# Performance work log

Hardware: AMD Instinct MI355X
Metric: run time of the kernel (lower is better)

The kernel has to match this reference:

```python
import jax, jax.numpy as jnp
import numpy as np


def feature_map(x):
    # phi(x) = elu(x) + 1 (ensures positivity)
    return jax.nn.elu(x) + 1.0


def setup_inputs() -> dict:
    key = jax.random.key(0)
    k0, k1, k2, k3 = jax.random.split(key, 4)
    B, T, d_model, D = 4, 4096, 1024, 128
    x = jax.random.normal(k0, (B, T, d_model), dtype=jnp.float32)
    s = 1.0 / np.sqrt(d_model)
    Wq = jax.random.normal(k1, (d_model, D), dtype=jnp.float32) * s
    Wk = jax.random.normal(k2, (d_model, D), dtype=jnp.float32) * s
    Wv = jax.random.normal(k3, (d_model, D), dtype=jnp.float32) * s
    return {"x": x, "Wq": Wq, "Wk": Wk, "Wv": Wv}


def _causal_linear_attention(phi_q, phi_k, v):
    # phi_q, phi_k: [B,T,D]; v: [B,T,Dv]
    B, T, D = phi_q.shape
    Dv = v.shape[-1]
    # time-major for scan: [T,B,D]
    qT = jnp.swapaxes(phi_q, 0, 1)
    kT = jnp.swapaxes(phi_k, 0, 1)
    vT = jnp.swapaxes(v, 0, 1)

    def step(carry, inp):
        kv, ks = carry                       # kv: [B,D,Dv], ks: [B,D]
        qt, kt, vt = inp                     # each [B,D] / [B,Dv]
        kv = kv + kt[:, :, None] * vt[:, None, :]   # k_t^T v_t outer product
        ks = ks + kt
        num = jnp.einsum('bd,bdv->bv', qt, kv)      # [B,Dv]
        den = jnp.einsum('bd,bd->b', qt, ks)[:, None]
        return (kv, ks), num / den

    init = (jnp.zeros((B, D, Dv), phi_q.dtype), jnp.zeros((B, D), phi_q.dtype))
    _, outT = jax.lax.scan(step, init, (qT, kT, vT))  # outT: [T,B,Dv]
    return jnp.swapaxes(outT, 0, 1)


def reference(x, Wq, Wk, Wv):
    q = x @ Wq
    k = x @ Wk
    v = x @ Wv
    phi_q = feature_map(q)
    phi_k = feature_map(k)
    # dropout is identity in eval mode
    return _causal_linear_attention(phi_q, phi_k, v)
```

## Files before the change

### kernel.cpp

```cpp
#include <hip/hip_runtime.h>

#define DMODEL 1024
#define DHEAD 128
#define CHUNK 128
#define NCHUNK 32

typedef __attribute__((ext_vector_type(4))) float f32x4;
typedef __attribute__((ext_vector_type(8))) short bf16x8;

__device__ __forceinline__ unsigned short f2bf(float f) {
  union { float f; unsigned u; } v; v.f = f;
  unsigned r = v.u + 0x7FFF + ((v.u >> 16) & 1);
  return (unsigned short)(r >> 16);
}
__device__ __forceinline__ float bf2f(unsigned short h) {
  union { unsigned u; float f; } v; v.u = ((unsigned)h) << 16;
  return v.f;
}
__device__ __forceinline__ unsigned cvtpk(float lo, float hi) {
  unsigned r;
  asm("v_cvt_pk_bf16_f32 %0, %1, %2" : "=v"(r) : "v"(lo), "v"(hi));
  return r;
}
__device__ __forceinline__ void gload16(const void* g, void* l) {
  __builtin_amdgcn_global_load_lds(
      (const __attribute__((address_space(1))) unsigned int*)g,
      (__attribute__((address_space(3))) unsigned int*)l, 16, 0, 0);
}

__global__ __launch_bounds__(256) void transpose_w_kernel(
    const float* __restrict__ Wq, const float* __restrict__ Wk,
    const float* __restrict__ Wv, unsigned short* __restrict__ WT) {
  int id = blockIdx.x * 256 + threadIdx.x;
  int w = id >> 17;
  int rem = id & 131071;
  int n = rem >> 10;
  int k = rem & 1023;
  const float* W = (w == 0) ? Wq : (w == 1) ? Wk : Wv;
  WT[id] = f2bf(W[(size_t)k * DHEAD + n]);
}

__global__ __launch_bounds__(256) void proj_kernel(
    const float* __restrict__ x, const unsigned short* __restrict__ WT,
    unsigned short* __restrict__ phiQ, unsigned short* __restrict__ phiK,
    unsigned short* __restrict__ Vb) {
  const int bid = blockIdx.x;
  const int xcd = bid & 7;
  const int slot = bid >> 3;
  const int n0 = (slot & 1) << 6;
  const int m0 = ((xcd << 6) | (slot >> 1)) << 5;

  __shared__ float xs[32][64];
  __shared__ unsigned short wl[3][64][64];

  const int tid = threadIdx.x;
  const int wave = tid >> 6;
  const int lane = tid & 63;
  const int lrow = lane & 15, kgrp = lane >> 4;

  f32x4 acc[3][2];
#pragma unroll
  for (int w3 = 0; w3 < 3; ++w3)
#pragma unroll
    for (int mi = 0; mi < 2; ++mi) acc[w3][mi] = (f32x4)0.0f;

  for (int kk = 0; kk < DMODEL; kk += 64) {
    if (kk) __syncthreads();
#pragma unroll
    for (int i = 0; i < 2; ++i) {
      int instr = i * 4 + wave;
      int row = instr * 4 + (lane >> 4);
      int slotc = lane & 15;
      int gcol = (slotc ^ (row & 7)) << 2;
      gload16(&x[(size_t)(m0 + row) * DMODEL + kk + gcol],
              (char*)xs + instr * 1024);
    }
#pragma unroll
    for (int i = 0; i < 6; ++i) {
      int j = i * 4 + wave;
      int w3 = j >> 3;
      int jj = j & 7;
      int row = jj * 8 + (lane >> 3);
      int slotc = lane & 7;
      int gcol = (slotc ^ (row & 7)) << 3;
      gload16(&WT[(size_t)w3 * (DHEAD * DMODEL) + (size_t)(n0 + row) * DMODEL + kk + gcol],
              (char*)wl + w3 * 8192 + jj * 1024);
    }
    __syncthreads();

#pragma unroll
    for (int ks2 = 0; ks2 < 2; ++ks2) {
      bf16x8 af[2];
#pragma unroll
      for (int mi = 0; mi < 2; ++mi) {
        int arow = mi * 16 + lrow;
        int s0 = ks2 * 8 + kgrp * 2;
        const float4 f0 = *reinterpret_cast<const float4*>(
            &xs[arow][(s0 ^ (arow & 7)) << 2]);
        const float4 f1 = *reinterpret_cast<const float4*>(
            &xs[arow][((s0 + 1) ^ (arow & 7)) << 2]);
        union { unsigned u[4]; bf16x8 v; } p;
        p.u[0] = cvtpk(f0.x, f0.y);
        p.u[1] = cvtpk(f0.z, f0.w);
        p.u[2] = cvtpk(f1.x, f1.y);
        p.u[3] = cvtpk(f1.z, f1.w);
        af[mi] = p.v;
      }
#pragma unroll
      for (int w3 = 0; w3 < 3; ++w3) {
        int brow = wave * 16 + lrow;
        int bs = ks2 * 4 + kgrp;
        bf16x8 bf = *reinterpret_cast<const bf16x8*>(
            &wl[w3][brow][(bs ^ (brow & 7)) << 3]);
#pragma unroll
        for (int mi = 0; mi < 2; ++mi)
          acc[w3][mi] = __builtin_amdgcn_mfma_f32_16x16x32_bf16(af[mi], bf, acc[w3][mi], 0, 0, 0);
      }
    }
  }
#pragma unroll
  for (int w3 = 0; w3 < 3; ++w3) {
    unsigned short* outp = (w3 == 0) ? phiQ : (w3 == 1) ? phiK : Vb;
#pragma unroll
    for (int mi = 0; mi < 2; ++mi)
#pragma unroll
      for (int r = 0; r < 4; ++r) {
        int row = m0 + mi * 16 + kgrp * 4 + r;
        int col = n0 + wave * 16 + lrow;
        float v = acc[w3][mi][r];
        if (w3 < 2) v = (v > 0.0f) ? (v + 1.0f) : __expf(v);
        outp[(size_t)row * DHEAD + col] = f2bf(v);
      }
  }
}

__global__ __launch_bounds__(256) void chunkkv_kernel(
    const unsigned short* __restrict__ phiK, const unsigned short* __restrict__ Vb,
    float* __restrict__ KVc, float* __restrict__ ksc) {
  const int c = blockIdx.x;
  const int yv = blockIdx.y;
  const size_t base = (size_t)c * CHUNK * DHEAD;
  __shared__ unsigned short kt[128][136];
  __shared__ unsigned short vt[64][136];
  __shared__ float csum[2][128];
  const int tid = threadIdx.x;
  const int wave = tid >> 6, lane = tid & 63;
  const int lrow = lane & 15, kgrp = lane >> 4;

  {
    int t = tid & 127, dp = tid >> 7;
#pragma unroll
    for (int i = 0; i < 8; ++i) {
      int d0 = (dp + 2 * i) * 8;
      uint4 k4 = *reinterpret_cast<const uint4*>(&phiK[base + (size_t)t * DHEAD + d0]);
      const unsigned short* kp = reinterpret_cast<const unsigned short*>(&k4);
#pragma unroll
      for (int j = 0; j < 8; ++j) kt[d0 + j][t] = kp[j];
    }
#pragma unroll
    for (int i = 0; i < 4; ++i) {
      int dl = (dp + 2 * i) * 8;
      uint4 v4 = *reinterpret_cast<const uint4*>(
          &Vb[base + (size_t)t * DHEAD + yv * 64 + dl]);
      const unsigned short* vp = reinterpret_cast<const unsigned short*>(&v4);
#pragma unroll
      for (int j = 0; j < 8; ++j) vt[dl + j][t] = vp[j];
    }
  }
  __syncthreads();

  f32x4 acc[8];
#pragma unroll
  for (int j = 0; j < 8; ++j) acc[j] = (f32x4)0.0f;
#pragma unroll
  for (int ks = 0; ks < 4; ++ks) {
    int t0 = ks * 32 + kgrp * 8;
    bf16x8 afrag = *reinterpret_cast<const bf16x8*>(&vt[wave * 16 + lrow][t0]);
#pragma unroll
    for (int tc = 0; tc < 8; ++tc) {
      bf16x8 bfrag = *reinterpret_cast<const bf16x8*>(&kt[tc * 16 + lrow][t0]);
      acc[tc] = __builtin_amdgcn_mfma_f32_16x16x32_bf16(afrag, bfrag, acc[tc], 0, 0, 0);
    }
  }
  float* KVout = KVc + (size_t)c * (DHEAD * DHEAD);
#pragma unroll
  for (int tc = 0; tc < 8; ++tc)
#pragma unroll
    for (int r = 0; r < 4; ++r) {
      int dv = yv * 64 + wave * 16 + kgrp * 4 + r;
      int d = tc * 16 + lrow;
      KVout[dv * DHEAD + d] = acc[tc][r];
    }
  if (yv == 0) {
    int d = tid & 127, hh = tid >> 7;
    float s = 0.0f;
    for (int t = hh * 64; t < hh * 64 + 64; ++t) s += bf2f(kt[d][t]);
    csum[hh][d] = s;
    __syncthreads();
    if (tid < 128) ksc[(size_t)c * DHEAD + tid] = csum[0][tid] + csum[1][tid];
  }
}

__global__ __launch_bounds__(256) void prefix_kernel(
    const float* __restrict__ KVc, const float* __restrict__ ksc,
    unsigned short* __restrict__ KVp, float* __restrict__ ksp) {
  if (blockIdx.x < 256) {
    int id = blockIdx.x * 256 + threadIdx.x;
    int b = id >> 14;
    int e = id & 16383;
    size_t base = (size_t)b * NCHUNK * 16384 + e;
    float acc = 0.0f;
    for (int c = 0; c < NCHUNK; ++c) {
      KVp[base + (size_t)c * 16384] = f2bf(acc);
      acc += KVc[base + (size_t)c * 16384];
    }
  } else {
    for (int i = threadIdx.x; i < 512; i += 256) {
      int b = i >> 7, d = i & 127;
      size_t base = (size_t)b * NCHUNK * DHEAD + d;
      float acc = 0.0f;
      for (int c = 0; c < NCHUNK; ++c) {
        ksp[base + (size_t)c * DHEAD] = acc;
        acc += ksc[base + (size_t)c * DHEAD];
      }
    }
  }
}

__global__ __launch_bounds__(256) void out_kernel(
    const unsigned short* __restrict__ phiQ, const unsigned short* __restrict__ phiK,
    const unsigned short* __restrict__ Vb, const unsigned short* __restrict__ KVp,
    const float* __restrict__ ksp, float* __restrict__ outp) {
  const int c = blockIdx.x;
  const int h = blockIdx.y;
  const size_t kvbase = (size_t)c * CHUNK * DHEAD;
  const size_t qbase = kvbase + (size_t)h * 64 * DHEAD;
  __shared__ unsigned short qb[64][136];
  __shared__ unsigned short kb[128][136];
  __shared__ unsigned short vt[128][136];
  __shared__ float dsum[4][64];
  __shared__ float ks_l[128];
  const int tid = threadIdx.x;
  const int wave = tid >> 6, lane = tid & 63;
  const int lrow = lane & 15, kgrp = lane >> 4;

#pragma unroll
  for (int it = 0; it < 4; ++it) {
    int idx = it * 256 + tid;
    int t = idx >> 4;
    int d0 = (idx & 15) << 3;
    *reinterpret_cast<uint4*>(&qb[t][d0]) =
        *reinterpret_cast<const uint4*>(&phiQ[qbase + (size_t)t * DHEAD + d0]);
  }
  if (tid < 128) ks_l[tid] = ksp[(size_t)c * DHEAD + tid];
  if (h == 0) {
#pragma unroll
    for (int it = 0; it < 4; ++it) {
      int idx = it * 256 + tid;
      int t = idx >> 4;
      int d0 = (idx & 15) << 3;
      *reinterpret_cast<uint4*>(&kb[t][d0]) =
          *reinterpret_cast<const uint4*>(&phiK[kvbase + (size_t)t * DHEAD + d0]);
    }
    int t = tid & 63, dp = tid >> 6;
#pragma unroll
    for (int i = 0; i < 4; ++i) {
      int d0 = (dp + 4 * i) * 8;
      uint4 v4 = *reinterpret_cast<const uint4*>(&Vb[kvbase + (size_t)t * DHEAD + d0]);
      const unsigned short* vp = reinterpret_cast<const unsigned short*>(&v4);
#pragma unroll
      for (int j = 0; j < 8; ++j) vt[d0 + j][t] = vp[j];
    }
  } else {
#pragma unroll
    for (int it = 0; it < 8; ++it) {
      int idx = it * 256 + tid;
      int t = idx >> 4;
      int d0 = (idx & 15) << 3;
      *reinterpret_cast<uint4*>(&kb[t][d0]) =
          *reinterpret_cast<const uint4*>(&phiK[kvbase + (size_t)t * DHEAD + d0]);
    }
    int t = tid & 127, dp = tid >> 7;
#pragma unroll
    for (int i = 0; i < 8; ++i) {
      int d0 = (dp + 2 * i) * 8;
      uint4 v4 = *reinterpret_cast<const uint4*>(&Vb[kvbase + (size_t)t * DHEAD + d0]);
      const unsigned short* vp = reinterpret_cast<const unsigned short*>(&v4);
#pragma unroll
      for (int j = 0; j < 8; ++j) vt[d0 + j][t] = vp[j];
    }
  }
  __syncthreads();

  if (h == 0) {
    f32x4 sa[4];
#pragma unroll
    for (int i = 0; i < 4; ++i) sa[i] = (f32x4)0.0f;
#pragma unroll
    for (int ks = 0; ks < 4; ++ks) {
      int d0 = ks * 32 + kgrp * 8;
      bf16x8 af = *reinterpret_cast<const bf16x8*>(&qb[wave * 16 + lrow][d0]);
#pragma unroll
      for (int tc = 0; tc < 4; ++tc) {
        bf16x8 bf = *reinterpret_cast<const bf16x8*>(&kb[tc * 16 + lrow][d0]);
        sa[tc] = __builtin_amdgcn_mfma_f32_16x16x32_bf16(af, bf, sa[tc], 0, 0, 0);
      }
    }
    __syncthreads();
#pragma unroll
    for (int tc = 0; tc < 4; ++tc)
#pragma unroll
      for (int r = 0; r < 4; ++r) {
        int trow = wave * 16 + kgrp * 4 + r;
        int s = tc * 16 + lrow;
        kb[trow][s] = f2bf((s <= trow) ? sa[tc][r] : 0.0f);
      }
  } else {
    f32x4 sa[8];
#pragma unroll
    for (int i = 0; i < 8; ++i) sa[i] = (f32x4)0.0f;
#pragma unroll
    for (int ks = 0; ks < 4; ++ks) {
      int d0 = ks * 32 + kgrp * 8;
      bf16x8 af = *reinterpret_cast<const bf16x8*>(&qb[wave * 16 + lrow][d0]);
#pragma unroll
      for (int tc = 0; tc < 8; ++tc) {
        bf16x8 bf = *reinterpret_cast<const bf16x8*>(&kb[tc * 16 + lrow][d0]);
        sa[tc] = __builtin_amdgcn_mfma_f32_16x16x32_bf16(af, bf, sa[tc], 0, 0, 0);
      }
    }
    __syncthreads();
#pragma unroll
    for (int tc = 0; tc < 8; ++tc)
#pragma unroll
      for (int r = 0; r < 4; ++r) {
        int trow = wave * 16 + kgrp * 4 + r;
        int s = tc * 16 + lrow;
        kb[trow][s] = f2bf((s <= 64 + trow) ? sa[tc][r] : 0.0f);
      }
  }
  __syncthreads();

  {
    int t = tid & 63, h4 = tid >> 6;
    float s = 0.0f;
    if (h4 < 2) {
      if (h4 == 0 || h == 1) {
        for (int j = h4 * 64; j < h4 * 64 + 64; ++j) s += bf2f(kb[t][j]);
      }
    } else {
      for (int j = (h4 - 2) * 64; j < (h4 - 2) * 64 + 64; ++j)
        s += bf2f(qb[t][j]) * ks_l[j];
    }
    dsum[h4][t] = s;
  }

  f32x4 acc[8];
#pragma unroll
  for (int i = 0; i < 8; ++i) acc[i] = (f32x4)0.0f;
  {
    const int nks = (h == 0) ? 2 : 4;
    for (int ks = 0; ks < nks; ++ks) {
      int t0 = ks * 32 + kgrp * 8;
      bf16x8 af = *reinterpret_cast<const bf16x8*>(&kb[wave * 16 + lrow][t0]);
#pragma unroll
      for (int tc = 0; tc < 8; ++tc) {
        bf16x8 bf = *reinterpret_cast<const bf16x8*>(&vt[tc * 16 + lrow][t0]);
        acc[tc] = __builtin_amdgcn_mfma_f32_16x16x32_bf16(af, bf, acc[tc], 0, 0, 0);
      }
    }
  }
  __syncthreads();

#pragma unroll
  for (int it = 0; it < 8; ++it) {
    int idx = it * 256 + tid;
    int dv = idx >> 4;
    int d0 = (idx & 15) << 3;
    *reinterpret_cast<uint4*>(&vt[dv][d0]) =
        *reinterpret_cast<const uint4*>(&KVp[(size_t)c * 16384 + (size_t)dv * DHEAD + d0]);
  }
  __syncthreads();

#pragma unroll
  for (int ks = 0; ks < 4; ++ks) {
    int d0 = ks * 32 + kgrp * 8;
    bf16x8 af = *reinterpret_cast<const bf16x8*>(&qb[wave * 16 + lrow][d0]);
#pragma unroll
    for (int tc = 0; tc < 8; ++tc) {
      bf16x8 bf = *reinterpret_cast<const bf16x8*>(&vt[tc * 16 + lrow][d0]);
      acc[tc] = __builtin_amdgcn_mfma_f32_16x16x32_bf16(af, bf, acc[tc], 0, 0, 0);
    }
  }

#pragma unroll
  for (int tc = 0; tc < 8; ++tc)
#pragma unroll
    for (int r = 0; r < 4; ++r) {
      int trow = wave * 16 + kgrp * 4 + r;
      int dv = tc * 16 + lrow;
      float den = dsum[0][trow] + dsum[1][trow] + dsum[2][trow] + dsum[3][trow];
      outp[qbase + (size_t)trow * DHEAD + dv] = acc[tc][r] / den;
    }
}

extern "C" void kernel_launch(void* const* d_in, const int* in_sizes, int n_in,
                              void* d_out, int out_size, void* d_ws, size_t ws_size,
                              hipStream_t stream) {
  const float* x  = (const float*)d_in[0];
  const float* Wq = (const float*)d_in[1];
  const float* Wk = (const float*)d_in[2];
  const float* Wv = (const float*)d_in[3];
  float* out = (float*)d_out;
  char* ws = (char*)d_ws;
  unsigned short* phiQ = (unsigned short*)(ws + 0);
  unsigned short* phiK = (unsigned short*)(ws + 4194304);
  unsigned short* Vb   = (unsigned short*)(ws + 8388608);
  unsigned short* WT   = (unsigned short*)(ws + 12582912);
  float*          KVc  = (float*)(ws + 13369344);
  unsigned short* KVp  = (unsigned short*)(ws + 21757952);
  float*          ksc  = (float*)(ws + 25952256);
  float*          ksp  = (float*)(ws + 26017792);

  transpose_w_kernel<<<1536, 256, 0, stream>>>(Wq, Wk, Wv, WT);
  proj_kernel<<<1024, 256, 0, stream>>>(x, WT, phiQ, phiK, Vb);
  chunkkv_kernel<<<dim3(128, 2), 256, 0, stream>>>(phiK, Vb, KVc, ksc);
  prefix_kernel<<<257, 256, 0, stream>>>(KVc, ksc, KVp, ksp);
  out_kernel<<<dim3(128, 2), 256, 0, stream>>>(phiQ, phiK, Vb, KVp, ksp, out);
}
```

Measured before the change: 55.55 us.

## Double-buffer x tiles and load weights directly into registers in projection GEMM

The projection kernel now double-buffers the x tile in shared memory and prefetches the next k-step while computing the current one, using explicit vmcnt waits and barriers. Weight fragments are no longer staged through LDS; each lane loads its bf16 B-operand straight from global memory into a double-buffered register array. This aims to hide global load latency and cut LDS traffic and barriers. In exchange it uses more registers and relies on hand-counted vmcnt values, and the weight loads are uncoalesced per-lane 16-byte reads.

```diff
diff --git a/kernel.cpp b/kernel.cpp
--- a/kernel.cpp
+++ b/kernel.cpp
@@ -50,43 +50,61 @@
   const int n0 = (slot & 1) << 6;
   const int m0 = ((xcd << 6) | (slot >> 1)) << 5;
 
-  __shared__ float xs[32][64];
-  __shared__ unsigned short wl[3][64][64];
+  __shared__ float xs[2][32][64];
 
   const int tid = threadIdx.x;
   const int wave = tid >> 6;
   const int lane = tid & 63;
   const int lrow = lane & 15, kgrp = lane >> 4;
 
+  const unsigned short* wrow =
+      WT + (size_t)(n0 + wave * 16 + lrow) * DMODEL + kgrp * 8;
+
   f32x4 acc[3][2];
 #pragma unroll
   for (int w3 = 0; w3 < 3; ++w3)
 #pragma unroll
     for (int mi = 0; mi < 2; ++mi) acc[w3][mi] = (f32x4)0.0f;
 
-  for (int kk = 0; kk < DMODEL; kk += 64) {
-    if (kk) __syncthreads();
-#pragma unroll
-    for (int i = 0; i < 2; ++i) {
-      int instr = i * 4 + wave;
-      int row = instr * 4 + (lane >> 4);
-      int slotc = lane & 15;
-      int gcol = (slotc ^ (row & 7)) << 2;
-      gload16(&x[(size_t)(m0 + row) * DMODEL + kk + gcol],
-              (char*)xs + instr * 1024);
-    }
-#pragma unroll
-    for (int i = 0; i < 6; ++i) {
-      int j = i * 4 + wave;
-      int w3 = j >> 3;
-      int jj = j & 7;
-      int row = jj * 8 + (lane >> 3);
-      int slotc = lane & 7;
-      int gcol = (slotc ^ (row & 7)) << 3;
-      gload16(&WT[(size_t)w3 * (DHEAD * DMODEL) + (size_t)(n0 + row) * DMODEL + kk + gcol],
-              (char*)wl + w3 * 8192 + jj * 1024);
-    }
-    __syncthreads();
+  bf16x8 wreg[2][3][2];
+
+#define STAGE_X(T)                                                        \
+  {                                                                       \
+    _Pragma("unroll")                                                     \
+    for (int i = 0; i < 2; ++i) {                                         \
+      int instr = i * 4 + wave;                                           \
+      int row = instr * 4 + (lane >> 4);                                  \
+      int slotc = lane & 15;                                              \
+      int gcol = (slotc ^ (row & 7)) << 2;                                \
+      gload16(&x[(size_t)(m0 + row) * DMODEL + (T) * 64 + gcol],          \
+              (char*)xs[(T) & 1] + instr * 1024);                         \
+    }                                                                     \
+  }
+#define LOAD_W(T)                                                         \
+  {                                                                       \
+    _Pragma("unroll")                                                     \
+    for (int w3 = 0; w3 < 3; ++w3)                                        \
+      _Pragma("unroll")                                                   \
+      for (int ks2 = 0; ks2 < 2; ++ks2)                                   \
+        wreg[(T) & 1][w3][ks2] = *reinterpret_cast<const bf16x8*>(        \
+            wrow + (size_t)w3 * (DHEAD * DMODEL) + (T) * 64 + ks2 * 32);  \
+  }
+
+  STAGE_X(0);
+  LOAD_W(0);
+
+#pragma unroll
+  for (int t = 0; t < 16; ++t) {
+    if (t < 15) {
+      STAGE_X(t + 1);
+      LOAD_W(t + 1);
+      asm volatile("s_waitcnt vmcnt(8)" ::: "memory");
+    } else {
+      asm volatile("s_waitcnt vmcnt(0)" ::: "memory");
+    }
+    __builtin_amdgcn_sched_barrier(0);
+    __builtin_amdgcn_s_barrier();
+    __builtin_amdgcn_sched_barrier(0);
 
 #pragma unroll
     for (int ks2 = 0; ks2 < 2; ++ks2) {
@@ -96,9 +114,9 @@
         int arow = mi * 16 + lrow;
         int s0 = ks2 * 8 + kgrp * 2;
         const float4 f0 = *reinterpret_cast<const float4*>(
-            &xs[arow][(s0 ^ (arow & 7)) << 2]);
+            &xs[t & 1][arow][(s0 ^ (arow & 7)) << 2]);
         const float4 f1 = *reinterpret_cast<const float4*>(
-            &xs[arow][((s0 + 1) ^ (arow & 7)) << 2]);
+            &xs[t & 1][arow][((s0 + 1) ^ (arow & 7)) << 2]);
         union { unsigned u[4]; bf16x8 v; } p;
         p.u[0] = cvtpk(f0.x, f0.y);
         p.u[1] = cvtpk(f0.z, f0.w);
@@ -107,17 +125,18 @@
         af[mi] = p.v;
       }
 #pragma unroll
-      for (int w3 = 0; w3 < 3; ++w3) {
-        int brow = wave * 16 + lrow;
-        int bs = ks2 * 4 + kgrp;
-        bf16x8 bf = *reinterpret_cast<const bf16x8*>(
-            &wl[w3][brow][(bs ^ (brow & 7)) << 3]);
+      for (int w3 = 0; w3 < 3; ++w3)
 #pragma unroll
         for (int mi = 0; mi < 2; ++mi)
-          acc[w3][mi] = __builtin_amdgcn_mfma_f32_16x16x32_bf16(af[mi], bf, acc[w3][mi], 0, 0, 0);
-      }
-    }
-  }
+          acc[w3][mi] = __builtin_amdgcn_mfma_f32_16x16x32_bf16(
+              af[mi], wreg[t & 1][w3][ks2], acc[w3][mi], 0, 0, 0);
+    }
+    __builtin_amdgcn_sched_barrier(0);
+    __builtin_amdgcn_s_barrier();
+  }
+#undef STAGE_X
+#undef LOAD_W
+
 #pragma unroll
   for (int w3 = 0; w3 < 3; ++w3) {
     unsigned short* outp = (w3 == 0) ? phiQ : (w3 == 1) ? phiK : Vb;
```

Measured after the change: 80.06 us. 1.44x slower.

## Restructure projection GEMM: per-weight grid, 64x128 tiles, register-prefetched bf16 x in LDS

Applied to the files above, without the earlier changes.

The projection kernel now launches one grid slice per weight (Q/K/V) with 64-row by 128-column tiles and two waves per block. Previously each block computed all three projections on a 32x64 tile. x is loaded into registers one K-step ahead, converted to bf16 once, and stored in LDS. This removes the repeated fp32-to-bf16 conversion and halves the LDS footprint for x, with the aim of better MFMA-to-load ratio and overlapping global loads with compute. The cost is that each x tile is now read three times, once per weight, plus higher register pressure from 16 accumulators and 16 prefetch registers per thread.

```diff
diff --git a/kernel.cpp b/kernel.cpp
--- a/kernel.cpp
+++ b/kernel.cpp
@@ -40,98 +40,107 @@
   WT[id] = f2bf(W[(size_t)k * DHEAD + n]);
 }
 
-__global__ __launch_bounds__(256) void proj_kernel(
+__global__ __launch_bounds__(128) void proj_kernel(
     const float* __restrict__ x, const unsigned short* __restrict__ WT,
     unsigned short* __restrict__ phiQ, unsigned short* __restrict__ phiK,
     unsigned short* __restrict__ Vb) {
-  const int bid = blockIdx.x;
-  const int xcd = bid & 7;
-  const int slot = bid >> 3;
-  const int n0 = (slot & 1) << 6;
-  const int m0 = ((xcd << 6) | (slot >> 1)) << 5;
-
-  __shared__ float xs[32][64];
-  __shared__ unsigned short wl[3][64][64];
+  const int which = blockIdx.y;
+  const unsigned short* Wt = WT + (size_t)which * (DHEAD * DMODEL);
+  unsigned short* outp = (which == 0) ? phiQ : (which == 1) ? phiK : Vb;
+  const int m0 = blockIdx.x * 64;
+
+  __shared__ unsigned short xs[64][128];
+  __shared__ unsigned short ws[128][128];
 
   const int tid = threadIdx.x;
   const int wave = tid >> 6;
   const int lane = tid & 63;
   const int lrow = lane & 15, kgrp = lane >> 4;
 
-  f32x4 acc[3][2];
-#pragma unroll
-  for (int w3 = 0; w3 < 3; ++w3)
-#pragma unroll
-    for (int mi = 0; mi < 2; ++mi) acc[w3][mi] = (f32x4)0.0f;
-
-  for (int kk = 0; kk < DMODEL; kk += 64) {
-    if (kk) __syncthreads();
-#pragma unroll
-    for (int i = 0; i < 2; ++i) {
-      int instr = i * 4 + wave;
+  f32x4 acc[2][8];
+#pragma unroll
+  for (int i = 0; i < 2; ++i)
+#pragma unroll
+    for (int j = 0; j < 8; ++j) acc[i][j] = (f32x4)0.0f;
+
+  float4 xr[16];
+
+#define LOADX(T)                                                           \
+  {                                                                        \
+    _Pragma("unroll")                                                      \
+    for (int i = 0; i < 16; ++i) {                                         \
+      int c = i * 128 + tid;                       \
+      int row = c >> 5;                                                    \
+      int col4 = c & 31;                                                   \
+      xr[i] = *reinterpret_cast<const float4*>(                            \
+          &x[(size_t)(m0 + row) * DMODEL + (T) * 128 + col4 * 4]);         \
+    }                                                                      \
+  }
+#define WRITEX()                                                           \
+  {                                                                        \
+    _Pragma("unroll")                                                      \
+    for (int i = 0; i < 16; ++i) {                                         \
+      int c = i * 128 + tid;                                               \
+      int row = c >> 5;                                                    \
+      int col4 = c & 31;                                                   \
+      int sl = (col4 >> 1) ^ ((row & 7) << 1);                             \
+      uint2 b;                                                             \
+      b.x = cvtpk(xr[i].x, xr[i].y);                                       \
+      b.y = cvtpk(xr[i].z, xr[i].w);                                       \
+      *reinterpret_cast<uint2*>(                                           \
+          (char*)&xs[row][0] + sl * 16 + (col4 & 1) * 8) = b;              \
+    }                                                                      \
+  }
+
+  LOADX(0);
+  for (int t = 0; t < 8; ++t) {
+    if (t) __syncthreads();
+#pragma unroll
+    for (int i = 0; i < 16; ++i) {
+      int instr = i * 2 + wave;
       int row = instr * 4 + (lane >> 4);
       int slotc = lane & 15;
-      int gcol = (slotc ^ (row & 7)) << 2;
-      gload16(&x[(size_t)(m0 + row) * DMODEL + kk + gcol],
-              (char*)xs + instr * 1024);
-    }
-#pragma unroll
-    for (int i = 0; i < 6; ++i) {
-      int j = i * 4 + wave;
-      int w3 = j >> 3;
-      int jj = j & 7;
-      int row = jj * 8 + (lane >> 3);
-      int slotc = lane & 7;
-      int gcol = (slotc ^ (row & 7)) << 3;
-      gload16(&WT[(size_t)w3 * (DHEAD * DMODEL) + (size_t)(n0 + row) * DMODEL + kk + gcol],
-              (char*)wl + w3 * 8192 + jj * 1024);
-    }
+      int sl = slotc ^ ((row & 7) << 1);
+      gload16(&Wt[(size_t)row * DMODEL + t * 128 + sl * 8],
+              (char*)ws + instr * 1024);
+    }
+    WRITEX();
     __syncthreads();
-
-#pragma unroll
-    for (int ks2 = 0; ks2 < 2; ++ks2) {
+    if (t < 7) LOADX(t + 1);
+#pragma unroll
+    for (int ks2 = 0; ks2 < 4; ++ks2) {
       bf16x8 af[2];
 #pragma unroll
       for (int mi = 0; mi < 2; ++mi) {
-        int arow = mi * 16 + lrow;
-        int s0 = ks2 * 8 + kgrp * 2;
-        const float4 f0 = *reinterpret_cast<const float4*>(
-            &xs[arow][(s0 ^ (arow & 7)) << 2]);
-        const float4 f1 = *reinterpret_cast<const float4*>(
-            &xs[arow][((s0 + 1) ^ (arow & 7)) << 2]);
-        union { unsigned u[4]; bf16x8 v; } p;
-        p.u[0] = cvtpk(f0.x, f0.y);
-        p.u[1] = cvtpk(f0.z, f0.w);
-        p.u[2] = cvtpk(f1.x, f1.y);
-        p.u[3] = cvtpk(f1.z, f1.w);
-        af[mi] = p.v;
-      }
-#pragma unroll
-      for (int w3 = 0; w3 < 3; ++w3) {
-        int brow = wave * 16 + lrow;
-        int bs = ks2 * 4 + kgrp;
-        bf16x8 bf = *reinterpret_cast<const bf16x8*>(
-            &wl[w3][brow][(bs ^ (brow & 7)) << 3]);
-#pragma unroll
-        for (int mi = 0; mi < 2; ++mi)
-          acc[w3][mi] = __builtin_amdgcn_mfma_f32_16x16x32_bf16(af[mi], bf, acc[w3][mi], 0, 0, 0);
-      }
-    }
-  }
-#pragma unroll
-  for (int w3 = 0; w3 < 3; ++w3) {
-    unsigned short* outp = (w3 == 0) ? phiQ : (w3 == 1) ? phiK : Vb;
-#pragma unroll
-    for (int mi = 0; mi < 2; ++mi)
+        int arow = wave * 32 + mi * 16 + lrow;
+        int sl = (ks2 * 4 + kgrp) ^ ((arow & 7) << 1);
+        af[mi] = *reinterpret_cast<const bf16x8*>((char*)&xs[arow][0] + sl * 16);
+      }
+#pragma unroll
+      for (int tc = 0; tc < 8; ++tc) {
+        int brow = tc * 16 + lrow;
+        int sl = (ks2 * 4 + kgrp) ^ ((brow & 7) << 1);
+        bf16x8 bf = *reinterpret_cast<const bf16x8*>((char*)&ws[brow][0] + sl * 16);
+        acc[0][tc] = __builtin_amdgcn_mfma_f32_16x16x32_bf16(af[0], bf, acc[0][tc], 0, 0, 0);
+        acc[1][tc] = __builtin_amdgcn_mfma_f32_16x16x32_bf16(af[1], bf, acc[1][tc], 0, 0, 0);
+      }
+    }
+  }
+#undef LOADX
+#undef WRITEX
+
+#pragma unroll
+  for (int mi = 0; mi < 2; ++mi)
+#pragma unroll
+    for (int tc = 0; tc < 8; ++tc)
 #pragma unroll
       for (int r = 0; r < 4; ++r) {
-        int row = m0 + mi * 16 + kgrp * 4 + r;
-        int col = n0 + wave * 16 + lrow;
-        float v = acc[w3][mi][r];
-        if (w3 < 2) v = (v > 0.0f) ? (v + 1.0f) : __expf(v);
+        int row = m0 + wave * 32 + mi * 16 + kgrp * 4 + r;
+        int col = tc * 16 + lrow;
+        float v = acc[mi][tc][r];
+        if (which < 2) v = (v > 0.0f) ? (v + 1.0f) : __expf(v);
         outp[(size_t)row * DHEAD + col] = f2bf(v);
       }
-  }
 }
 
 __global__ __launch_bounds__(256) void chunkkv_kernel(
@@ -423,7 +432,7 @@
   float*          ksp  = (float*)(ws + 26017792);
 
   transpose_w_kernel<<<1536, 256, 0, stream>>>(Wq, Wk, Wv, WT);
-  proj_kernel<<<1024, 256, 0, stream>>>(x, WT, phiQ, phiK, Vb);
+  proj_kernel<<<dim3(256, 3), 128, 0, stream>>>(x, WT, phiQ, phiK, Vb);
   chunkkv_kernel<<<dim3(128, 2), 256, 0, stream>>>(phiK, Vb, KVc, ksc);
   prefix_kernel<<<257, 256, 0, stream>>>(KVc, ksc, KVp, ksp);
   out_kernel<<<dim3(128, 2), 256, 0, stream>>>(phiQ, phiK, Vb, KVp, ksp, out);
```

Result: slower. 73.50 us (+32.3%).

## Enlarge projection tile to 64 rows and load x directly into registers

Applied to the files above, without the earlier changes.

The projection GEMM now uses 64x64 output tiles per block (512 blocks instead of 1024), with each wave owning 16 rows and all 64 columns for each of Q/K/V. The x tile is read straight from global memory into registers and converted to bf16 there, so x no longer goes through shared memory. Weights are staged in K-steps of 128 with a new XOR swizzle. This cuts the weight traffic per output and removes LDS round-trips for x. In exchange it raises register pressure (48 accumulator vectors), and the uncoalesced-style row loads of x may expose global latency because they are not overlapped with compute.

```diff
diff --git a/kernel.cpp b/kernel.cpp
--- a/kernel.cpp
+++ b/kernel.cpp
@@ -45,89 +45,79 @@
     unsigned short* __restrict__ phiQ, unsigned short* __restrict__ phiK,
     unsigned short* __restrict__ Vb) {
   const int bid = blockIdx.x;
-  const int xcd = bid & 7;
-  const int slot = bid >> 3;
-  const int n0 = (slot & 1) << 6;
-  const int m0 = ((xcd << 6) | (slot >> 1)) << 5;
-
-  __shared__ float xs[32][64];
-  __shared__ unsigned short wl[3][64][64];
+  const int nh = (bid >> 3) & 1;
+  const int mt = (bid & 7) + ((bid >> 4) << 3);
+  const int n0 = nh << 6;
+  const int m0 = mt << 6;
+
+  __shared__ unsigned short wl[3][64][128];
 
   const int tid = threadIdx.x;
   const int wave = tid >> 6;
   const int lane = tid & 63;
   const int lrow = lane & 15, kgrp = lane >> 4;
 
-  f32x4 acc[3][2];
+  const float* xrow = &x[(size_t)(m0 + wave * 16 + lrow) * DMODEL + kgrp * 8];
+
+  f32x4 acc[3][4];
 #pragma unroll
   for (int w3 = 0; w3 < 3; ++w3)
 #pragma unroll
-    for (int mi = 0; mi < 2; ++mi) acc[w3][mi] = (f32x4)0.0f;
-
-  for (int kk = 0; kk < DMODEL; kk += 64) {
-    if (kk) __syncthreads();
-#pragma unroll
-    for (int i = 0; i < 2; ++i) {
+    for (int nt = 0; nt < 4; ++nt) acc[w3][nt] = (f32x4)0.0f;
+
+  for (int t = 0; t < 8; ++t) {
+    if (t) __syncthreads();
+#pragma unroll
+    for (int i = 0; i < 12; ++i) {
       int instr = i * 4 + wave;
-      int row = instr * 4 + (lane >> 4);
-      int slotc = lane & 15;
-      int gcol = (slotc ^ (row & 7)) << 2;
-      gload16(&x[(size_t)(m0 + row) * DMODEL + kk + gcol],
-              (char*)xs + instr * 1024);
-    }
-#pragma unroll
-    for (int i = 0; i < 6; ++i) {
-      int j = i * 4 + wave;
-      int w3 = j >> 3;
-      int jj = j & 7;
-      int row = jj * 8 + (lane >> 3);
-      int slotc = lane & 7;
-      int gcol = (slotc ^ (row & 7)) << 3;
-      gload16(&WT[(size_t)w3 * (DHEAD * DMODEL) + (size_t)(n0 + row) * DMODEL + kk + gcol],
-              (char*)wl + w3 * 8192 + jj * 1024);
+      int w3 = instr >> 4;
+      int rowblk = instr & 15;
+      int row = rowblk * 4 + (lane >> 4);
+      int slot = lane & 15;
+      int gcol = (slot ^ ((row & 7) << 1)) << 3;
+      gload16(&WT[(size_t)w3 * (DHEAD * DMODEL) + (size_t)(n0 + row) * DMODEL + t * 128 + gcol],
+              (char*)wl + instr * 1024);
+    }
+    float4 xa[8];
+#pragma unroll
+    for (int ks = 0; ks < 4; ++ks) {
+      xa[2 * ks]     = *reinterpret_cast<const float4*>(xrow + t * 128 + ks * 32);
+      xa[2 * ks + 1] = *reinterpret_cast<const float4*>(xrow + t * 128 + ks * 32 + 4);
     }
     __syncthreads();
 
 #pragma unroll
-    for (int ks2 = 0; ks2 < 2; ++ks2) {
-      bf16x8 af[2];
-#pragma unroll
-      for (int mi = 0; mi < 2; ++mi) {
-        int arow = mi * 16 + lrow;
-        int s0 = ks2 * 8 + kgrp * 2;
-        const float4 f0 = *reinterpret_cast<const float4*>(
-            &xs[arow][(s0 ^ (arow & 7)) << 2]);
-        const float4 f1 = *reinterpret_cast<const float4*>(
-            &xs[arow][((s0 + 1) ^ (arow & 7)) << 2]);
-        union { unsigned u[4]; bf16x8 v; } p;
-        p.u[0] = cvtpk(f0.x, f0.y);
-        p.u[1] = cvtpk(f0.z, f0.w);
-        p.u[2] = cvtpk(f1.x, f1.y);
-        p.u[3] = cvtpk(f1.z, f1.w);
-        af[mi] = p.v;
-      }
-#pragma unroll
-      for (int w3 = 0; w3 < 3; ++w3) {
-        int brow = wave * 16 + lrow;
-        int bs = ks2 * 4 + kgrp;
-        bf16x8 bf = *reinterpret_cast<const bf16x8*>(
-            &wl[w3][brow][(bs ^ (brow & 7)) << 3]);
-#pragma unroll
-        for (int mi = 0; mi < 2; ++mi)
-          acc[w3][mi] = __builtin_amdgcn_mfma_f32_16x16x32_bf16(af[mi], bf, acc[w3][mi], 0, 0, 0);
-      }
-    }
-  }
+    for (int ks = 0; ks < 4; ++ks) {
+      union { unsigned u[4]; bf16x8 v; } p;
+      p.u[0] = cvtpk(xa[2 * ks].x, xa[2 * ks].y);
+      p.u[1] = cvtpk(xa[2 * ks].z, xa[2 * ks].w);
+      p.u[2] = cvtpk(xa[2 * ks + 1].x, xa[2 * ks + 1].y);
+      p.u[3] = cvtpk(xa[2 * ks + 1].z, xa[2 * ks + 1].w);
+      bf16x8 af = p.v;
+      int s = ks * 4 + kgrp;
+#pragma unroll
+      for (int w3 = 0; w3 < 3; ++w3)
+#pragma unroll
+        for (int nt = 0; nt < 4; ++nt) {
+          int brow = nt * 16 + lrow;
+          int sl = s ^ ((brow & 7) << 1);
+          bf16x8 bf = *reinterpret_cast<const bf16x8*>(
+              (char*)wl + w3 * 16384 + brow * 256 + sl * 16);
+          acc[w3][nt] = __builtin_amdgcn_mfma_f32_16x16x32_bf16(af, bf, acc[w3][nt], 0, 0, 0);
+        }
+    }
+  }
+
 #pragma unroll
   for (int w3 = 0; w3 < 3; ++w3) {
     unsigned short* outp = (w3 == 0) ? phiQ : (w3 == 1) ? phiK : Vb;
 #pragma unroll
-    for (int mi = 0; mi < 2; ++mi)
+    for (int nt = 0; nt < 4; ++nt)
 #pragma unroll
       for (int r = 0; r < 4; ++r) {
-        int row = m0 + mi * 16 + kgrp * 4 + r;
-        int col = n0 + wave * 16 + lrow;
-        float v = acc[w3][mi][r];
+        int row = m0 + wave * 16 + kgrp * 4 + r;
+        int col = n0 + nt * 16 + lrow;
+        float v = acc[w3][nt][r];
         if (w3 < 2) v = (v > 0.0f) ? (v + 1.0f) : __expf(v);
         outp[(size_t)row * DHEAD + col] = f2bf(v);
       }
@@ -423,7 +413,7 @@
   float*          ksp  = (float*)(ws + 26017792);
 
   transpose_w_kernel<<<1536, 256, 0, stream>>>(Wq, Wk, Wv, WT);
-  proj_kernel<<<1024, 256, 0, stream>>>(x, WT, phiQ, phiK, Vb);
+  proj_kernel<<<512, 256, 0, stream>>>(x, WT, phiQ, phiK, Vb);
   chunkkv_kernel<<<dim3(128, 2), 256, 0, stream>>>(phiK, Vb, KVc, ksc);
   prefix_kernel<<<257, 256, 0, stream>>>(KVc, ksc, KVp, ksp);
   out_kernel<<<dim3(128, 2), 256, 0, stream>>>(phiQ, phiK, Vb, KVp, ksp, out);
```

Result: slower. 60.99 us (+9.8%).
